# Optimization experiments

Hardware: AMD Instinct MI355X
Metric: run time of the kernel (lower is better)

Reference implementation:

```python
import jax, jax.numpy as jnp
import numpy as np

N = 50000        # nodes
E = 800000       # edges (avg degree 16)
F_IN = 128       # in_features
F_OUT = 64       # out_features per head
HEADS = 4        # SparseGATConv default n_heads
ALPHA = 0.01     # LeakyReLU negative slope (SparseGATConv default alpha)


def setup_inputs() -> dict:
    key = jax.random.key(0)
    ks = jax.random.split(key, 6)
    x = jax.random.normal(ks[0], (N, F_IN), dtype=jnp.float32)
    edge_index = jax.random.randint(ks[1], (2, E), 0, N, dtype=jnp.int64)
    # xavier-normal-ish init, gain 1.414 as in the torch module
    W_heads = jax.random.normal(ks[2], (HEADS, F_IN, F_OUT), dtype=jnp.float32) * (1.414 / np.sqrt(F_IN))
    attn_heads = jax.random.normal(ks[3], (HEADS, 2 * F_OUT, 1), dtype=jnp.float32) * 0.1
    W_out = jax.random.normal(ks[4], (HEADS * F_OUT, F_OUT), dtype=jnp.float32) * (1.414 / np.sqrt(HEADS * F_OUT))
    attn_out = jax.random.normal(ks[5], (2 * F_OUT, 1), dtype=jnp.float32) * 0.1
    return {"x": x, "edge_index": edge_index, "W_heads": W_heads,
            "attn_heads": attn_heads, "W_out": W_out, "attn_out": attn_out}


def _sp_gat_layer(x, src, dst, W, attn, concat):
    """SpGraphAttentionLayer.forward: dense x @ W, edge attention scores,
    sparse row-softmax over COO adjacency, sparse-mm aggregation."""
    h = x @ W                                   # (N, d)
    d = h.shape[1]
    # cat(h[src], h[dst]) @ attn  ==  (h@a1)[src] + (h@a2)[dst]  (avoids (E,2d) concat)
    s1 = (h @ attn[:d]).squeeze(-1)             # (N,)
    s2 = (h @ attn[d:]).squeeze(-1)             # (N,)
    scores = -jax.nn.leaky_relu(s1[src] + s2[dst], negative_slope=ALPHA)  # (E,)
    # torch.sparse.softmax(dim=1): softmax over existing entries in each row (src)
    row_max = jax.ops.segment_max(scores, src, num_segments=N)
    ex = jnp.exp(scores - row_max[src])
    denom = jax.ops.segment_sum(ex, src, num_segments=N)
    a = ex / denom[src]                         # (E,) edge attention weights
    # sparse.mm: out[i] = sum_{e: src[e]=i} a[e] * h[dst[e]]
    out = jax.ops.segment_sum(a[:, None] * h[dst], src, num_segments=N)  # (N, d)
    return jax.nn.elu(out) if concat else out


def reference(x, edge_index, W_heads, attn_heads, W_out, attn_out):
    src, dst = edge_index[0], edge_index[1]
    # multi-head GAT layers (concat=True), then out_att on concatenated features
    heads_out = jax.vmap(lambda W, a: _sp_gat_layer(x, src, dst, W, a, True))(W_heads, attn_heads)  # (H, N, F_OUT)
    hcat = jnp.transpose(heads_out, (1, 0, 2)).reshape(N, HEADS * F_OUT)  # matches torch.cat(dim=1) head order
    return _sp_gat_layer(hcat, src, dst, W_out, attn_out, False)          # (N, F_OUT)
```

## Files before the change

kernel.cpp:

```cpp
#include <hip/hip_runtime.h>

typedef unsigned short u16;
typedef _Float16 f16;
typedef __attribute__((ext_vector_type(8))) _Float16 f16x8;
typedef __attribute__((ext_vector_type(2))) _Float16 f16x2;
typedef __attribute__((ext_vector_type(4))) float f32x4;

__device__ inline float nlrelu(float z) { return (z > 0.f) ? -z : -0.01f * z; }
__device__ inline float4 score4(float4 a, float4 b) {
    return make_float4(nlrelu(a.x + b.x), nlrelu(a.y + b.y), nlrelu(a.z + b.z), nlrelu(a.w + b.w));
}
__device__ inline unsigned packdup(float w) {
    f16x2 p = (f16x2){(f16)w, (f16)w};
    return __builtin_bit_cast(unsigned, p);
}

__global__ __launch_bounds__(256) void k_initcnt(const float* __restrict__ Wh, const float* __restrict__ Wo,
                       f16* __restrict__ B1, f16* __restrict__ B2,
                       const int* __restrict__ src, int* __restrict__ counts, int* __restrict__ pos,
                       int E, int N) {
    const int b = blockIdx.x;
    if (b < 128) {
        int i = b * 256 + threadIdx.x;
        int j = i & 7, lane = (i >> 3) & 63, kg = (i >> 9) & 3, nt = i >> 11;
        int n = nt * 16 + (lane & 15);
        int k = kg * 32 + ((lane >> 4) << 3) + j;
        B1[i] = (f16)Wh[(n >> 6) * (128 * 64) + k * 64 + (n & 63)];
    } else if (b < 192) {
        int i = (b - 128) * 256 + threadIdx.x;
        int j = i & 7, lane = (i >> 3) & 63, kg = (i >> 9) & 7, nt = i >> 12;
        int n = nt * 16 + (lane & 15);
        int k = kg * 32 + ((lane >> 4) << 3) + j;
        B2[i] = (f16)Wo[k * 64 + n];
    } else {
        const int base = (b - 192) * 1024 + threadIdx.x;
#pragma unroll
        for (int j = 0; j < 4; j++) {
            int e = base + j * 256;
            if (e < E) {
                int s = src[e];
                s = ((unsigned)s < (unsigned)N) ? s : 0;
                pos[e] = atomicAdd(&counts[s], 1);
            }
        }
    }
}

__global__ __launch_bounds__(1024) void scan_ticket(const int* __restrict__ counts, int* __restrict__ rowst,
                                                    int* __restrict__ cursor, int n) {
    const int t = threadIdx.x, lane = t & 63, w = t >> 6;
    __shared__ int wsum[16];
    __shared__ int sh_base;
    int i = blockIdx.x * 1024 + t;
    int v = (i < n) ? counts[i] : 0;
    int orig = v;
    for (int d = 1; d < 64; d <<= 1) { int x = __shfl_up(v, d); if (lane >= d) v += x; }
    if (lane == 63) wsum[w] = v;
    __syncthreads();
    if (t == 0) {
        int acc = 0;
        for (int j = 0; j < 16; j++) { int tmp = wsum[j]; wsum[j] = acc; acc += tmp; }
        sh_base = atomicAdd(cursor, acc);
    }
    __syncthreads();
    if (i < n) rowst[i] = sh_base + wsum[w] + (v - orig);
}

__global__ __launch_bounds__(256) void scatter_noat(const int* __restrict__ src, const int* __restrict__ dst,
                                                    const int* __restrict__ rowst, const int* __restrict__ pos,
                                                    int* __restrict__ edged, int E, int N) {
    const int base = blockIdx.x * 1024 + threadIdx.x;
#pragma unroll
    for (int j = 0; j < 4; j++) {
        int e = base + j * 256;
        if (e < E) {
            int s = src[e];
            s = ((unsigned)s < (unsigned)N) ? s : 0;
            int d = dst[e];
            d = ((unsigned)d < (unsigned)N) ? d : 0;
            edged[rowst[s] + pos[e]] = d;
        }
    }
}

__global__ __launch_bounds__(256) void gemm1_f16(const float* __restrict__ X, const f16* __restrict__ B1,
        const float* __restrict__ attnH,
        f16* __restrict__ H1, float* __restrict__ s1, float* __restrict__ s2, int M) {
    const int lane = threadIdx.x & 63, wave = threadIdx.x >> 6;
    const int row0 = (blockIdx.x * 4 + wave) * 16;
    if (row0 >= M) return;
    const int mrow = row0 + (lane & 15);
    const int koff = (lane >> 4) * 8;
    const float* aptr = X + (size_t)mrow * 128 + koff;

    f32x4 acc[16];
#pragma unroll
    for (int c = 0; c < 16; c++) acc[c] = (f32x4){0.f, 0.f, 0.f, 0.f};

#pragma unroll
    for (int kg = 0; kg < 4; kg++) {
        float av[8];
        *(float4*)av       = *(const float4*)(aptr + kg * 32);
        *(float4*)(av + 4) = *(const float4*)(aptr + kg * 32 + 4);
        f16x8 a;
#pragma unroll
        for (int j = 0; j < 8; j++) a[j] = (f16)av[j];
#pragma unroll
        for (int nt = 0; nt < 16; nt++) {
            const size_t bidx = (size_t)(((nt << 2) + kg) * 64 + lane) * 8;
            f16x8 bfr = *(const f16x8*)(B1 + bidx);
            acc[nt] = __builtin_amdgcn_mfma_f32_16x16x32_f16(a, bfr, acc[nt], 0, 0, 0);
        }
    }
    const int rbase = (lane >> 4) * 4;
    const int colq = lane & 15;
#pragma unroll
    for (int h = 0; h < 4; h++) {
        float s1a[4] = {0.f, 0.f, 0.f, 0.f}, s2a[4] = {0.f, 0.f, 0.f, 0.f};
#pragma unroll
        for (int q = 0; q < 4; q++) {
            const int nt = h * 4 + q;
            const int col = nt * 16 + colq;
            const float a1v = attnH[h * 128 + (col & 63)];
            const float a2v = attnH[h * 128 + 64 + (col & 63)];
#pragma unroll
            for (int r = 0; r < 4; r++) {
                float c = acc[nt][r];
                H1[(size_t)(row0 + rbase + r) * 256 + col] = (f16)c;
                s1a[r] += c * a1v;
                s2a[r] += c * a2v;
            }
        }
#pragma unroll
        for (int off = 1; off < 16; off <<= 1)
#pragma unroll
            for (int r = 0; r < 4; r++) {
                s1a[r] += __shfl_xor(s1a[r], off);
                s2a[r] += __shfl_xor(s2a[r], off);
            }
        if (colq == 0)
#pragma unroll
            for (int r = 0; r < 4; r++) {
                s1[(size_t)(row0 + rbase + r) * 4 + h] = s1a[r];
                s2[(size_t)(row0 + rbase + r) * 4 + h] = s2a[r];
            }
    }
}

__global__ __launch_bounds__(256) void gemm2_f16(const f16* __restrict__ Hc, const f16* __restrict__ B2,
        const float* __restrict__ attnO,
        f16* __restrict__ H2, float* __restrict__ s1b, float* __restrict__ s2b, int M) {
    const int lane = threadIdx.x & 63, wave = threadIdx.x >> 6;
    const int row0 = (blockIdx.x * 4 + wave) * 16;
    if (row0 >= M) return;
    const int mrow = row0 + (lane & 15);
    const int koff = (lane >> 4) * 8;
    const f16* ap = Hc + (size_t)mrow * 256 + koff;

    f32x4 acc[4];
#pragma unroll
    for (int c = 0; c < 4; c++) acc[c] = (f32x4){0.f, 0.f, 0.f, 0.f};

#pragma unroll
    for (int kg = 0; kg < 8; kg++) {
        f16x8 a = *(const f16x8*)(ap + kg * 32);
#pragma unroll
        for (int nt = 0; nt < 4; nt++) {
            const size_t bidx = (size_t)(((nt << 3) + kg) * 64 + lane) * 8;
            f16x8 bfr = *(const f16x8*)(B2 + bidx);
            acc[nt] = __builtin_amdgcn_mfma_f32_16x16x32_f16(a, bfr, acc[nt], 0, 0, 0);
        }
    }
    const int rbase = (lane >> 4) * 4;
    const int colq = lane & 15;
    float s1a[4] = {0.f, 0.f, 0.f, 0.f}, s2a[4] = {0.f, 0.f, 0.f, 0.f};
#pragma unroll
    for (int nt = 0; nt < 4; nt++) {
        const int col = nt * 16 + colq;
        const float a1v = attnO[col];
        const float a2v = attnO[64 + col];
#pragma unroll
        for (int r = 0; r < 4; r++) {
            float c = acc[nt][r];
            H2[(size_t)(row0 + rbase + r) * 64 + col] = (f16)c;
            s1a[r] += c * a1v;
            s2a[r] += c * a2v;
        }
    }
#pragma unroll
    for (int off = 1; off < 16; off <<= 1)
#pragma unroll
        for (int r = 0; r < 4; r++) {
            s1a[r] += __shfl_xor(s1a[r], off);
            s2a[r] += __shfl_xor(s2a[r], off);
        }
    if (colq == 0)
#pragma unroll
        for (int r = 0; r < 4; r++) {
            s1b[row0 + rbase + r] = s1a[r];
            s2b[row0 + rbase + r] = s2a[r];
        }
}

__global__ __launch_bounds__(256) void agg_l1(const int* __restrict__ rowst, const int* __restrict__ cnt,
                                              const int* __restrict__ edged,
                                              const float* __restrict__ s1, const float* __restrict__ s2,
                                              const f16* __restrict__ H, f16* __restrict__ hcat, int N) {
    __shared__ unsigned wls[4][64][4];
    __shared__ int dls[4][64];
    const int t = threadIdx.x, lane = t & 63, wave = t >> 6;
    const int node = blockIdx.x * 4 + wave;
    if (node >= N) return;
    const int beg = rowst[node];
    const int deg = cnt[node];
    const int end = beg + deg;
    const int head = lane >> 4;
    f16* outp = hcat + (size_t)node * 256 + lane * 4;
    if (deg == 0) { *(uint2*)outp = make_uint2(0u, 0u); return; }
    const float4 s1v = *(const float4*)(s1 + (size_t)node * 4);

    float r0, r1, r2, r3;
    if (deg <= 64) {
        int d = 0;
        if (lane < deg) d = edged[beg + lane];
        dls[wave][lane] = d;
        float4 s2v = *(const float4*)(s2 + (size_t)d * 4);
        float4 sc = score4(s1v, s2v);
        if (lane >= deg) sc = make_float4(-3e38f, -3e38f, -3e38f, -3e38f);
        float4 m = sc;
#pragma unroll
        for (int off = 32; off > 0; off >>= 1) {
            m.x = fmaxf(m.x, __shfl_xor(m.x, off));
            m.y = fmaxf(m.y, __shfl_xor(m.y, off));
            m.z = fmaxf(m.z, __shfl_xor(m.z, off));
            m.w = fmaxf(m.w, __shfl_xor(m.w, off));
        }
        float4 ex = make_float4(0.f, 0.f, 0.f, 0.f);
        if (lane < deg) ex = make_float4(__expf(sc.x - m.x), __expf(sc.y - m.y),
                                         __expf(sc.z - m.z), __expf(sc.w - m.w));
        float4 sm = ex;
#pragma unroll
        for (int off = 32; off > 0; off >>= 1) {
            sm.x += __shfl_xor(sm.x, off);
            sm.y += __shfl_xor(sm.y, off);
            sm.z += __shfl_xor(sm.z, off);
            sm.w += __shfl_xor(sm.w, off);
        }
        wls[wave][lane][0] = packdup(ex.x / sm.x);
        wls[wave][lane][1] = packdup(ex.y / sm.y);
        wls[wave][lane][2] = packdup(ex.z / sm.z);
        wls[wave][lane][3] = packdup(ex.w / sm.w);
        f16x2 a01[4], a23[4];
#pragma unroll
        for (int j = 0; j < 4; j++) { a01[j] = (f16x2)(f16)0.f; a23[j] = (f16x2)(f16)0.f; }
        int e = 0;
        for (; e + 8 <= deg; e += 8) {
            uint2 raw[8];
#pragma unroll
            for (int j = 0; j < 8; j++)
                raw[j] = *(const uint2*)(H + (size_t)dls[wave][e + j] * 256 + lane * 4);
#pragma unroll
            for (int j = 0; j < 8; j++) {
                f16x2 lo = __builtin_bit_cast(f16x2, raw[j].x);
                f16x2 hi = __builtin_bit_cast(f16x2, raw[j].y);
                f16x2 w2 = __builtin_bit_cast(f16x2, wls[wave][e + j][head]);
                a01[j & 3] += w2 * lo;
                a23[j & 3] += w2 * hi;
            }
        }
        for (; e + 4 <= deg; e += 4) {
#pragma unroll
            for (int j = 0; j < 4; j++) {
                int dd = dls[wave][e + j];
                uint2 raw = *(const uint2*)(H + (size_t)dd * 256 + lane * 4);
                f16x2 lo = __builtin_bit_cast(f16x2, raw.x);
                f16x2 hi = __builtin_bit_cast(f16x2, raw.y);
                f16x2 w2 = __builtin_bit_cast(f16x2, wls[wave][e + j][head]);
                a01[j] += w2 * lo;
                a23[j] += w2 * hi;
            }
        }
        for (; e < deg; e++) {
            int dd = dls[wave][e];
            uint2 raw = *(const uint2*)(H + (size_t)dd * 256 + lane * 4);
            f16x2 lo = __builtin_bit_cast(f16x2, raw.x);
            f16x2 hi = __builtin_bit_cast(f16x2, raw.y);
            f16x2 w2 = __builtin_bit_cast(f16x2, wls[wave][e][head]);
            a01[0] += w2 * lo;
            a23[0] += w2 * hi;
        }
        r0 = (float)a01[0][0] + (float)a01[1][0] + (float)a01[2][0] + (float)a01[3][0];
        r1 = (float)a01[0][1] + (float)a01[1][1] + (float)a01[2][1] + (float)a01[3][1];
        r2 = (float)a23[0][0] + (float)a23[1][0] + (float)a23[2][0] + (float)a23[3][0];
        r3 = (float)a23[0][1] + (float)a23[1][1] + (float)a23[2][1] + (float)a23[3][1];
    } else {
        float4 m = make_float4(-3e38f, -3e38f, -3e38f, -3e38f);
        for (int e = beg + lane; e < end; e += 64) {
            int d = edged[e];
            float4 sc = score4(s1v, *(const float4*)(s2 + (size_t)d * 4));
            m.x = fmaxf(m.x, sc.x); m.y = fmaxf(m.y, sc.y); m.z = fmaxf(m.z, sc.z); m.w = fmaxf(m.w, sc.w);
        }
#pragma unroll
        for (int off = 32; off > 0; off >>= 1) {
            m.x = fmaxf(m.x, __shfl_xor(m.x, off));
            m.y = fmaxf(m.y, __shfl_xor(m.y, off));
            m.z = fmaxf(m.z, __shfl_xor(m.z, off));
            m.w = fmaxf(m.w, __shfl_xor(m.w, off));
        }
        float4 sm = make_float4(0.f, 0.f, 0.f, 0.f);
        for (int e = beg + lane; e < end; e += 64) {
            int d = edged[e];
            float4 sc = score4(s1v, *(const float4*)(s2 + (size_t)d * 4));
            sm.x += __expf(sc.x - m.x); sm.y += __expf(sc.y - m.y);
            sm.z += __expf(sc.z - m.z); sm.w += __expf(sc.w - m.w);
        }
#pragma unroll
        for (int off = 32; off > 0; off >>= 1) {
            sm.x += __shfl_xor(sm.x, off);
            sm.y += __shfl_xor(sm.y, off);
            sm.z += __shfl_xor(sm.z, off);
            sm.w += __shfl_xor(sm.w, off);
        }
        float4 inv = make_float4(1.f / sm.x, 1.f / sm.y, 1.f / sm.z, 1.f / sm.w);
        float4 acc = make_float4(0.f, 0.f, 0.f, 0.f);
        for (int e = beg; e < end; e++) {
            int dd = edged[e];
            float4 sc = score4(s1v, *(const float4*)(s2 + (size_t)dd * 4));
            float wv[4] = { __expf(sc.x - m.x) * inv.x, __expf(sc.y - m.y) * inv.y,
                            __expf(sc.z - m.z) * inv.z, __expf(sc.w - m.w) * inv.w };
            float w = (head == 0) ? wv[0] : (head == 1) ? wv[1] : (head == 2) ? wv[2] : wv[3];
            const f16* hp = H + (size_t)dd * 256 + lane * 4;
            acc.x += w * (float)hp[0]; acc.y += w * (float)hp[1];
            acc.z += w * (float)hp[2]; acc.w += w * (float)hp[3];
        }
        r0 = acc.x; r1 = acc.y; r2 = acc.z; r3 = acc.w;
    }
    r0 = (r0 > 0.f) ? r0 : (__expf(r0) - 1.f);
    r1 = (r1 > 0.f) ? r1 : (__expf(r1) - 1.f);
    r2 = (r2 > 0.f) ? r2 : (__expf(r2) - 1.f);
    r3 = (r3 > 0.f) ? r3 : (__expf(r3) - 1.f);
    f16x2 o0 = (f16x2){(f16)r0, (f16)r1};
    f16x2 o1 = (f16x2){(f16)r2, (f16)r3};
    *(uint2*)outp = make_uint2(__builtin_bit_cast(unsigned, o0), __builtin_bit_cast(unsigned, o1));
}

__global__ __launch_bounds__(256) void agg_l2(const int* __restrict__ rowst, const int* __restrict__ cnt,
                                              const int* __restrict__ edged,
                                              const float* __restrict__ s1, const float* __restrict__ s2,
                                              const f16* __restrict__ H, float* __restrict__ outp, int N) {
    __shared__ float wls[4][64];
    __shared__ int dls[4][64];
    const int t = threadIdx.x, lane = t & 63, wave = t >> 6;
    const int node = blockIdx.x * 4 + wave;
    if (node >= N) return;
    const int beg = rowst[node];
    const int deg = cnt[node];
    const int end = beg + deg;
    if (deg == 0) { outp[(size_t)node * 64 + lane] = 0.f; return; }
    const float s1v = s1[node];

    float acc = 0.f;
    if (deg <= 64) {
        int d = 0;
        if (lane < deg) d = edged[beg + lane];
        dls[wave][lane] = d;
        float z = s1v + s2[d];
        float sc = (lane < deg) ? nlrelu(z) : -3e38f;
        float m = sc;
#pragma unroll
        for (int off = 32; off > 0; off >>= 1) m = fmaxf(m, __shfl_xor(m, off));
        float ex = (lane < deg) ? __expf(sc - m) : 0.f;
        float sm = ex;
#pragma unroll
        for (int off = 32; off > 0; off >>= 1) sm += __shfl_xor(sm, off);
        wls[wave][lane] = ex / sm;
        int e = 0;
        for (; e + 4 <= deg; e += 4) {
            int d0 = dls[wave][e], d1 = dls[wave][e + 1], d2 = dls[wave][e + 2], d3 = dls[wave][e + 3];
            float h0 = (float)H[(size_t)d0 * 64 + lane];
            float h1 = (float)H[(size_t)d1 * 64 + lane];
            float h2 = (float)H[(size_t)d2 * 64 + lane];
            float h3 = (float)H[(size_t)d3 * 64 + lane];
            acc += wls[wave][e] * h0 + wls[wave][e + 1] * h1 + wls[wave][e + 2] * h2 + wls[wave][e + 3] * h3;
        }
        for (; e < deg; e++)
            acc += wls[wave][e] * (float)H[(size_t)dls[wave][e] * 64 + lane];
    } else {
        float m = -3e38f;
        for (int e = beg + lane; e < end; e += 64) {
            int d = edged[e];
            m = fmaxf(m, nlrelu(s1v + s2[d]));
        }
#pragma unroll
        for (int off = 32; off > 0; off >>= 1) m = fmaxf(m, __shfl_xor(m, off));
        float sm = 0.f;
        for (int e = beg + lane; e < end; e += 64) {
            int d = edged[e];
            sm += __expf(nlrelu(s1v + s2[d]) - m);
        }
#pragma unroll
        for (int off = 32; off > 0; off >>= 1) sm += __shfl_xor(sm, off);
        float inv = 1.f / sm;
        for (int e = beg; e < end; e++) {
            int dd = edged[e];
            float w = __expf(nlrelu(s1v + s2[dd]) - m) * inv;
            acc += w * (float)H[(size_t)dd * 64 + lane];
        }
    }
    outp[(size_t)node * 64 + lane] = acc;
}

extern "C" void kernel_launch(void* const* d_in, const int* in_sizes, int n_in,
                              void* d_out, int out_size, void* d_ws, size_t ws_size,
                              hipStream_t stream) {
    const float* x     = (const float*)d_in[0];
    const int*   ei    = (const int*)d_in[1];
    const float* Wh    = (const float*)d_in[2];
    const float* attnH = (const float*)d_in[3];
    const float* Wo    = (const float*)d_in[4];
    const float* attnO = (const float*)d_in[5];
    float* out         = (float*)d_out;

    const int N = in_sizes[0] / 128;
    const int E = in_sizes[1] / 2;
    const int* srcp = ei;
    const int* dstp = ei + E;

    char* base = (char*)d_ws;
    size_t off = 0;
    auto take = [&](size_t b) { void* p = base + off; off += (b + 255) & ~(size_t)255; return p; };
    f16*   B1     = (f16*)  take(32768 * 2);
    f16*   B2     = (f16*)  take(16384 * 2);
    int*   counts = (int*)  take((size_t)N * 4);
    int*   rowst  = (int*)  take((size_t)N * 4);
    int*   pos    = (int*)  take((size_t)E * 4);
    int*   edged  = (int*)  take((size_t)E * 4);
    int*   cursor = (int*)  take(256);
    float* s1     = (float*)take((size_t)N * 4 * 4);
    float* s2     = (float*)take((size_t)N * 4 * 4);
    float* s1b    = (float*)take((size_t)N * 4);
    float* s2b    = (float*)take((size_t)N * 4);
    f16*   H1     = (f16*)  take((size_t)N * 256 * 2);
    f16*   hcat   = (f16*)  take((size_t)N * 256 * 2);
    f16*   H2     = (f16*)  take((size_t)N * 64 * 2);

    hipMemsetAsync(counts, 0, (size_t)N * 4, stream);
    hipMemsetAsync(cursor, 0, 4, stream);

    const int eb4 = (E + 1023) / 1024;
    k_initcnt<<<192 + eb4, 256, 0, stream>>>(Wh, Wo, B1, B2, srcp, counts, pos, E, N);

    const int nb = (N + 1023) / 1024;
    scan_ticket<<<nb, 1024, 0, stream>>>(counts, rowst, cursor, N);

    scatter_noat<<<eb4, 256, 0, stream>>>(srcp, dstp, rowst, pos, edged, E, N);

    const int Gg = (N + 63) / 64;
    gemm1_f16<<<Gg, 256, 0, stream>>>(x, B1, attnH, H1, s1, s2, N);
    agg_l1<<<(N + 3) / 4, 256, 0, stream>>>(rowst, counts, edged, s1, s2, H1, hcat, N);
    gemm2_f16<<<Gg, 256, 0, stream>>>(hcat, B2, attnO, H2, s1b, s2b, N);
    agg_l2<<<(N + 3) / 4, 256, 0, stream>>>(rowst, counts, edged, s1b, s2b, H2, out, N);
}
```

Measured before the change: 257.2 us.

## Split each wave into two edge streams with wider gathers in aggregation kernels

In both aggregation kernels, for nodes with degree up to 64, each wave now handles two edges per iteration. Each half-wave loads a wider slice of a neighbour's row (16 bytes per lane in layer 1, 4 bytes in layer 2). The two halves are combined with a cross-half shuffle before the ELU and store. This halves the serial loop over neighbours and widens the gather loads, at the cost of one extra reduction step and idle upper lanes during the store. Separately, the cursor memset is folded into the first kernel to save a launch.

```diff
diff --git a/kernel.cpp b/kernel.cpp
--- a/kernel.cpp
+++ b/kernel.cpp
@@ -18,8 +18,9 @@
 __global__ __launch_bounds__(256) void k_initcnt(const float* __restrict__ Wh, const float* __restrict__ Wo,
                        f16* __restrict__ B1, f16* __restrict__ B2,
                        const int* __restrict__ src, int* __restrict__ counts, int* __restrict__ pos,
-                       int E, int N) {
+                       int* __restrict__ cursor, int E, int N) {
     const int b = blockIdx.x;
+    if (b == 0 && threadIdx.x == 0) *cursor = 0;
     if (b < 128) {
         int i = b * 256 + threadIdx.x;
         int j = i & 7, lane = (i >> 3) & 63, kg = (i >> 9) & 3, nt = i >> 11;
@@ -214,12 +215,12 @@
     const int beg = rowst[node];
     const int deg = cnt[node];
     const int end = beg + deg;
-    const int head = lane >> 4;
-    f16* outp = hcat + (size_t)node * 256 + lane * 4;
-    if (deg == 0) { *(uint2*)outp = make_uint2(0u, 0u); return; }
+    if (deg == 0) {
+        *(uint2*)(hcat + (size_t)node * 256 + lane * 4) = make_uint2(0u, 0u);
+        return;
+    }
     const float4 s1v = *(const float4*)(s1 + (size_t)node * 4);
 
-    float r0, r1, r2, r3;
     if (deg <= 64) {
         int d = 0;
         if (lane < deg) d = edged[beg + lane];
@@ -250,50 +251,52 @@
         wls[wave][lane][1] = packdup(ex.y / sm.y);
         wls[wave][lane][2] = packdup(ex.z / sm.z);
         wls[wave][lane][3] = packdup(ex.w / sm.w);
-        f16x2 a01[4], a23[4];
-#pragma unroll
-        for (int j = 0; j < 4; j++) { a01[j] = (f16x2)(f16)0.f; a23[j] = (f16x2)(f16)0.f; }
-        int e = 0;
-        for (; e + 8 <= deg; e += 8) {
-            uint2 raw[8];
-#pragma unroll
-            for (int j = 0; j < 8; j++)
-                raw[j] = *(const uint2*)(H + (size_t)dls[wave][e + j] * 256 + lane * 4);
-#pragma unroll
-            for (int j = 0; j < 8; j++) {
-                f16x2 lo = __builtin_bit_cast(f16x2, raw[j].x);
-                f16x2 hi = __builtin_bit_cast(f16x2, raw[j].y);
-                f16x2 w2 = __builtin_bit_cast(f16x2, wls[wave][e + j][head]);
-                a01[j & 3] += w2 * lo;
-                a23[j & 3] += w2 * hi;
-            }
-        }
-        for (; e + 4 <= deg; e += 4) {
+        const int h2 = lane >> 5;
+        const int p = lane & 31;
+        const int headp = p >> 3;
+        f16x2 a0[4], a1[4];
+#pragma unroll
+        for (int j = 0; j < 4; j++) { a0[j] = (f16x2)(f16)0.f; a1[j] = (f16x2)(f16)0.f; }
+        for (int e = 0; e < deg; e += 2) {
+            int ei = e + h2;
+            int dd = dls[wave][ei];
+            f16x2 w2 = __builtin_bit_cast(f16x2, wls[wave][ei][headp]);
+            uint4 raw = *(const uint4*)(H + (size_t)dd * 256 + p * 8);
+            if ((e >> 1) & 1) {
+                a1[0] += w2 * __builtin_bit_cast(f16x2, raw.x);
+                a1[1] += w2 * __builtin_bit_cast(f16x2, raw.y);
+                a1[2] += w2 * __builtin_bit_cast(f16x2, raw.z);
+                a1[3] += w2 * __builtin_bit_cast(f16x2, raw.w);
+            } else {
+                a0[0] += w2 * __builtin_bit_cast(f16x2, raw.x);
+                a0[1] += w2 * __builtin_bit_cast(f16x2, raw.y);
+                a0[2] += w2 * __builtin_bit_cast(f16x2, raw.z);
+                a0[3] += w2 * __builtin_bit_cast(f16x2, raw.w);
+            }
+        }
+        float r[8];
+#pragma unroll
+        for (int j = 0; j < 4; j++) {
+            r[2 * j]     = (float)a0[j][0] + (float)a1[j][0];
+            r[2 * j + 1] = (float)a0[j][1] + (float)a1[j][1];
+        }
+#pragma unroll
+        for (int k = 0; k < 8; k++) r[k] += __shfl_xor(r[k], 32);
+        if (lane < 32) {
+            uint4 o;
+            unsigned* op = &o.x;
 #pragma unroll
             for (int j = 0; j < 4; j++) {
-                int dd = dls[wave][e + j];
-                uint2 raw = *(const uint2*)(H + (size_t)dd * 256 + lane * 4);
-                f16x2 lo = __builtin_bit_cast(f16x2, raw.x);
-                f16x2 hi = __builtin_bit_cast(f16x2, raw.y);
-                f16x2 w2 = __builtin_bit_cast(f16x2, wls[wave][e + j][head]);
-                a01[j] += w2 * lo;
-                a23[j] += w2 * hi;
-            }
-        }
-        for (; e < deg; e++) {
-            int dd = dls[wave][e];
-            uint2 raw = *(const uint2*)(H + (size_t)dd * 256 + lane * 4);
-            f16x2 lo = __builtin_bit_cast(f16x2, raw.x);
-            f16x2 hi = __builtin_bit_cast(f16x2, raw.y);
-            f16x2 w2 = __builtin_bit_cast(f16x2, wls[wave][e][head]);
-            a01[0] += w2 * lo;
-            a23[0] += w2 * hi;
-        }
-        r0 = (float)a01[0][0] + (float)a01[1][0] + (float)a01[2][0] + (float)a01[3][0];
-        r1 = (float)a01[0][1] + (float)a01[1][1] + (float)a01[2][1] + (float)a01[3][1];
-        r2 = (float)a23[0][0] + (float)a23[1][0] + (float)a23[2][0] + (float)a23[3][0];
-        r3 = (float)a23[0][1] + (float)a23[1][1] + (float)a23[2][1] + (float)a23[3][1];
+                float v0 = r[2 * j], v1 = r[2 * j + 1];
+                v0 = (v0 > 0.f) ? v0 : (__expf(v0) - 1.f);
+                v1 = (v1 > 0.f) ? v1 : (__expf(v1) - 1.f);
+                f16x2 pk = (f16x2){(f16)v0, (f16)v1};
+                op[j] = __builtin_bit_cast(unsigned, pk);
+            }
+            *(uint4*)(hcat + (size_t)node * 256 + p * 8) = o;
+        }
     } else {
+        const int head = lane >> 4;
         float4 m = make_float4(-3e38f, -3e38f, -3e38f, -3e38f);
         for (int e = beg + lane; e < end; e += 64) {
             int d = edged[e];
@@ -333,15 +336,15 @@
             acc.x += w * (float)hp[0]; acc.y += w * (float)hp[1];
             acc.z += w * (float)hp[2]; acc.w += w * (float)hp[3];
         }
-        r0 = acc.x; r1 = acc.y; r2 = acc.z; r3 = acc.w;
-    }
-    r0 = (r0 > 0.f) ? r0 : (__expf(r0) - 1.f);
-    r1 = (r1 > 0.f) ? r1 : (__expf(r1) - 1.f);
-    r2 = (r2 > 0.f) ? r2 : (__expf(r2) - 1.f);
-    r3 = (r3 > 0.f) ? r3 : (__expf(r3) - 1.f);
-    f16x2 o0 = (f16x2){(f16)r0, (f16)r1};
-    f16x2 o1 = (f16x2){(f16)r2, (f16)r3};
-    *(uint2*)outp = make_uint2(__builtin_bit_cast(unsigned, o0), __builtin_bit_cast(unsigned, o1));
+        acc.x = (acc.x > 0.f) ? acc.x : (__expf(acc.x) - 1.f);
+        acc.y = (acc.y > 0.f) ? acc.y : (__expf(acc.y) - 1.f);
+        acc.z = (acc.z > 0.f) ? acc.z : (__expf(acc.z) - 1.f);
+        acc.w = (acc.w > 0.f) ? acc.w : (__expf(acc.w) - 1.f);
+        f16x2 o0 = (f16x2){(f16)acc.x, (f16)acc.y};
+        f16x2 o1 = (f16x2){(f16)acc.z, (f16)acc.w};
+        *(uint2*)(hcat + (size_t)node * 256 + lane * 4) =
+            make_uint2(__builtin_bit_cast(unsigned, o0), __builtin_bit_cast(unsigned, o1));
+    }
 }
 
 __global__ __launch_bounds__(256) void agg_l2(const int* __restrict__ rowst, const int* __restrict__ cnt,
@@ -359,7 +362,6 @@
     if (deg == 0) { outp[(size_t)node * 64 + lane] = 0.f; return; }
     const float s1v = s1[node];
 
-    float acc = 0.f;
     if (deg <= 64) {
         int d = 0;
         if (lane < deg) d = edged[beg + lane];
@@ -374,17 +376,21 @@
 #pragma unroll
         for (int off = 32; off > 0; off >>= 1) sm += __shfl_xor(sm, off);
         wls[wave][lane] = ex / sm;
-        int e = 0;
-        for (; e + 4 <= deg; e += 4) {
-            int d0 = dls[wave][e], d1 = dls[wave][e + 1], d2 = dls[wave][e + 2], d3 = dls[wave][e + 3];
-            float h0 = (float)H[(size_t)d0 * 64 + lane];
-            float h1 = (float)H[(size_t)d1 * 64 + lane];
-            float h2 = (float)H[(size_t)d2 * 64 + lane];
-            float h3 = (float)H[(size_t)d3 * 64 + lane];
-            acc += wls[wave][e] * h0 + wls[wave][e + 1] * h1 + wls[wave][e + 2] * h2 + wls[wave][e + 3] * h3;
-        }
-        for (; e < deg; e++)
-            acc += wls[wave][e] * (float)H[(size_t)dls[wave][e] * 64 + lane];
+        const int h2 = lane >> 5;
+        const int p = lane & 31;
+        float ax = 0.f, ay = 0.f;
+        for (int e = 0; e < deg; e += 2) {
+            int ei = e + h2;
+            float w = wls[wave][ei];
+            int dd = dls[wave][ei];
+            unsigned raw = *(const unsigned*)(H + (size_t)dd * 64 + p * 2);
+            f16x2 hv = __builtin_bit_cast(f16x2, raw);
+            ax += w * (float)hv[0];
+            ay += w * (float)hv[1];
+        }
+        ax += __shfl_xor(ax, 32);
+        ay += __shfl_xor(ay, 32);
+        if (lane < 32) *(float2*)(outp + (size_t)node * 64 + p * 2) = make_float2(ax, ay);
     } else {
         float m = -3e38f;
         for (int e = beg + lane; e < end; e += 64) {
@@ -401,13 +407,14 @@
 #pragma unroll
         for (int off = 32; off > 0; off >>= 1) sm += __shfl_xor(sm, off);
         float inv = 1.f / sm;
+        float acc = 0.f;
         for (int e = beg; e < end; e++) {
             int dd = edged[e];
             float w = __expf(nlrelu(s1v + s2[dd]) - m) * inv;
             acc += w * (float)H[(size_t)dd * 64 + lane];
         }
-    }
-    outp[(size_t)node * 64 + lane] = acc;
+        outp[(size_t)node * 64 + lane] = acc;
+    }
 }
 
 extern "C" void kernel_launch(void* const* d_in, const int* in_sizes, int n_in,
@@ -445,10 +452,9 @@
     f16*   H2     = (f16*)  take((size_t)N * 64 * 2);
 
     hipMemsetAsync(counts, 0, (size_t)N * 4, stream);
-    hipMemsetAsync(cursor, 0, 4, stream);
 
     const int eb4 = (E + 1023) / 1024;
-    k_initcnt<<<192 + eb4, 256, 0, stream>>>(Wh, Wo, B1, B2, srcp, counts, pos, E, N);
+    k_initcnt<<<192 + eb4, 256, 0, stream>>>(Wh, Wo, B1, B2, srcp, counts, pos, cursor, E, N);
 
     const int nb = (N + 1023) / 1024;
     scan_ticket<<<nb, 1024, 0, stream>>>(counts, rowst, cursor, N);
```

After: 258.1 us. No clear change (+0.4%).
